# Kernel optimization log

Hardware: AMD Instinct MI355X
Metric: run time of the kernel (lower is better)

The kernel has to match this reference:

```python
import jax, jax.numpy as jnp
import numpy as np

D = 1024       # d_model
H = 16         # num_heads
DK = D // H    # head dim (64)
DFF = 4096     # SwiGLU hidden dim
THETA = 10000.0
EPS = 1e-5
B, S = 2, 2048


def setup_inputs() -> dict:
    key = jax.random.key(0)
    ks = jax.random.split(key, 9)
    p = lambda k, shape: jax.random.normal(k, shape, dtype=jnp.float32) * 0.02
    return {
        "x": jax.random.normal(ks[0], (B, S, D), dtype=jnp.float32),
        "w_q": p(ks[1], (D, D)),   # Linear stores [out, in]
        "w_k": p(ks[2], (D, D)),
        "w_v": p(ks[3], (D, D)),
        "w_o": p(ks[4], (D, D)),
        "ln1_w": jnp.ones((D,), dtype=jnp.float32),
        "ln2_w": jnp.ones((D,), dtype=jnp.float32),
        "w1": p(ks[5], (DFF, D)),  # gate-in proj: d_model -> dff
        "w2": p(ks[6], (D, DFF)),  # down proj:    dff -> d_model
        "w3": p(ks[7], (DFF, D)),  # up proj:      d_model -> dff
    }


def _rmsnorm(x, w):
    xf = x.astype(jnp.float32)
    inv = jax.lax.rsqrt(jnp.mean(xf * xf, axis=-1, keepdims=True) + EPS)
    return (inv * xf * w).astype(x.dtype)


def _rope(x, pos):
    # x: [..., seq, DK]; pos: [seq]
    inv_freq = THETA ** (-(jnp.arange(0, DK, 2, dtype=jnp.float32) / DK))  # [DK/2]
    ang = pos.astype(jnp.float32)[:, None] * inv_freq                      # [seq, DK/2]
    cos, sin = jnp.cos(ang), jnp.sin(ang)
    xe, xo = x[..., ::2], x[..., 1::2]
    re = cos * xe - sin * xo
    ro = sin * xe + cos * xo
    return jnp.stack((re, ro), axis=-1).reshape(x.shape)  # interleave even/odd


def reference(x, w_q, w_k, w_v, w_o, ln1_w, ln2_w, w1, w2, w3):
    b, s, d = x.shape
    pos = jnp.arange(s)

    # --- attention sublayer ---
    h = _rmsnorm(x, ln1_w)
    def proj(w):  # [b,s,d] x [d,d] -> [b,H,s,DK]
        return jnp.einsum('bsd,ed->bse', h, w).reshape(b, s, H, DK).transpose(0, 2, 1, 3)
    q = _rope(proj(w_q), pos)
    k = _rope(proj(w_k), pos)
    v = proj(w_v)

    scores = jnp.einsum('bhqd,bhkd->bhqk', q, k) / (DK ** 0.5)
    causal = jnp.tril(jnp.ones((s, s), dtype=bool))
    scores = jnp.where(causal, scores, -jnp.inf)
    attn = jax.nn.softmax(scores, axis=-1)
    o = jnp.einsum('bhqk,bhkd->bhqd', attn, v).transpose(0, 2, 1, 3).reshape(b, s, d)
    x = x + jnp.einsum('bsd,ed->bse', o, w_o)

    # --- SwiGLU FFN sublayer ---
    h2 = _rmsnorm(x, ln2_w)
    u = jnp.einsum('bsd,fd->bsf', h2, w1)
    g = jnp.einsum('bsd,fd->bsf', h2, w3)
    ffn = jnp.einsum('bsf,df->bsd', u * jax.nn.sigmoid(u) * g, w2)
    return x + ffn
```

## Files before the change

kernel.cpp:

```cpp
#include <hip/hip_runtime.h>

typedef _Float16 half_t;
typedef _Float16 f16x8 __attribute__((ext_vector_type(8)));
typedef _Float16 f16x4 __attribute__((ext_vector_type(4)));
typedef _Float16 f16x2 __attribute__((ext_vector_type(2)));
typedef float fx4 __attribute__((ext_vector_type(4)));

typedef __attribute__((address_space(1))) const unsigned int as1_cuint;
typedef __attribute__((address_space(3))) unsigned int as3_uint;

__device__ __forceinline__ void gld16(const void* g, void* l) {
    __builtin_amdgcn_global_load_lds((as1_cuint*)g, (as3_uint*)l, 16, 0, 0);
}

#define L256(buf, half, sec) (lbase + (buf) * 65536 + (half) * 16384 + (sec) * 8192)

#define KT256(CUR)                                                            \
  {                                                                           \
    const int BO = (CUR) * 65536;                                             \
    const int st1 = (t < nt - 1), st2 = (t < nt - 2);                         \
    const int s1 = (t + 1) * 128, s2 = (t + 2) * 128;                         \
    f16x8 aLo[4][2], aHi[4][2], bA[2][2], bB[2][2];                           \
                                         \
    _Pragma("unroll") for (int mi = 0; mi < 4; mi++) {                        \
        aLo[mi][0] = *(const f16x8*)(aBase + BO + mi * 2048 + swz0);          \
        aLo[mi][1] = *(const f16x8*)(aBase + BO + mi * 2048 + swz1);          \
    }                                                                         \
    _Pragma("unroll") for (int ni = 0; ni < 2; ni++) {                        \
        bA[ni][0] = *(const f16x8*)(bBase + BO + ni * 2048 + swz0);           \
        bA[ni][1] = *(const f16x8*)(bBase + BO + ni * 2048 + swz1);           \
    }                                                                         \
    if (st1) { gld16(pB10 + s1, L256(1 - (CUR), 3, 0));                       \
               gld16(pB1h + s1, L256(1 - (CUR), 3, 1)); }                     \
    asm volatile("s_waitcnt lgkmcnt(8)" ::: "memory");                        \
    __builtin_amdgcn_s_barrier();                                             \
    asm volatile("s_waitcnt lgkmcnt(0)" ::: "memory");                        \
    __builtin_amdgcn_sched_barrier(0);                                        \
    __builtin_amdgcn_s_setprio(1);                                            \
    _Pragma("unroll") for (int kk = 0; kk < 2; kk++)                          \
      _Pragma("unroll") for (int mi = 0; mi < 4; mi++)                        \
        _Pragma("unroll") for (int ni = 0; ni < 2; ni++)                      \
          acc[mi][ni] = __builtin_amdgcn_mfma_f32_16x16x32_f16(aLo[mi][kk], bA[ni][kk], acc[mi][ni], 0, 0, 0); \
    __builtin_amdgcn_s_setprio(0);                                            \
    __builtin_amdgcn_s_barrier();                                             \
                                         \
    _Pragma("unroll") for (int ni = 0; ni < 2; ni++) {                        \
        bB[ni][0] = *(const f16x8*)(bBase + BO + (2 + ni) * 2048 + swz0);     \
        bB[ni][1] = *(const f16x8*)(bBase + BO + (2 + ni) * 2048 + swz1);     \
    }                                                                         \
    if (st2) { gld16(pA00 + s2, L256(CUR, 0, 0)); }                           \
    __builtin_amdgcn_s_barrier();                                             \
    asm volatile("s_waitcnt lgkmcnt(0)" ::: "memory");                        \
    __builtin_amdgcn_sched_barrier(0);                                        \
    __builtin_amdgcn_s_setprio(1);                                            \
    _Pragma("unroll") for (int kk = 0; kk < 2; kk++)                          \
      _Pragma("unroll") for (int mi = 0; mi < 4; mi++)                        \
        _Pragma("unroll") for (int ni = 0; ni < 2; ni++)                      \
          acc[mi][2 + ni] = __builtin_amdgcn_mfma_f32_16x16x32_f16(aLo[mi][kk], bB[ni][kk], acc[mi][2 + ni], 0, 0, 0); \
    __builtin_amdgcn_s_setprio(0);                                            \
    __builtin_amdgcn_s_barrier();                                             \
                                         \
    _Pragma("unroll") for (int mi = 0; mi < 4; mi++) {                        \
        aHi[mi][0] = *(const f16x8*)(aBase + BO + (4 + mi) * 2048 + swz0);    \
        aHi[mi][1] = *(const f16x8*)(aBase + BO + (4 + mi) * 2048 + swz1);    \
    }                                                                         \
    if (st2) { gld16(pB00 + s2, L256(CUR, 2, 0));                             \
               gld16(pB0h + s2, L256(CUR, 2, 1)); }                           \
    __builtin_amdgcn_s_barrier();                                             \
    asm volatile("s_waitcnt lgkmcnt(0)" ::: "memory");                        \
    __builtin_amdgcn_sched_barrier(0);                                        \
    __builtin_amdgcn_s_setprio(1);                                            \
    _Pragma("unroll") for (int kk = 0; kk < 2; kk++)                          \
      _Pragma("unroll") for (int mi = 0; mi < 4; mi++)                        \
        _Pragma("unroll") for (int ni = 0; ni < 2; ni++)                      \
          acc[4 + mi][2 + ni] = __builtin_amdgcn_mfma_f32_16x16x32_f16(aHi[mi][kk], bB[ni][kk], acc[4 + mi][2 + ni], 0, 0, 0); \
    __builtin_amdgcn_s_setprio(0);                                            \
    __builtin_amdgcn_s_barrier();                                             \
                                         \
    if (st2) { gld16(pA0h + s2, L256(CUR, 0, 1));                             \
               gld16(pA10 + s2, L256(CUR, 1, 0));                             \
               gld16(pA1h + s2, L256(CUR, 1, 1)); }                           \
    __builtin_amdgcn_s_barrier();                                             \
    __builtin_amdgcn_sched_barrier(0);                                        \
    __builtin_amdgcn_s_setprio(1);                                            \
    _Pragma("unroll") for (int kk = 0; kk < 2; kk++)                          \
      _Pragma("unroll") for (int mi = 0; mi < 4; mi++)                        \
        _Pragma("unroll") for (int ni = 0; ni < 2; ni++)                      \
          acc[4 + mi][ni] = __builtin_amdgcn_mfma_f32_16x16x32_f16(aHi[mi][kk], bA[ni][kk], acc[4 + mi][ni], 0, 0, 0); \
    __builtin_amdgcn_s_setprio(0);                                            \
    if (t < nt - 2)       { asm volatile("s_waitcnt vmcnt(6)" ::: "memory"); }\
    else if (t == nt - 2) { asm volatile("s_waitcnt vmcnt(0)" ::: "memory"); }\
    __builtin_amdgcn_s_barrier();                                             \
  }

#define PRO256()                                                              \
    gld16(pA00, L256(0, 0, 0));                                               \
    gld16(pB00, L256(0, 2, 0)); gld16(pB0h, L256(0, 2, 1));                   \
    gld16(pA0h, L256(0, 0, 1)); gld16(pA10, L256(0, 1, 0)); gld16(pA1h, L256(0, 1, 1)); \
    gld16(pB10, L256(0, 3, 0)); gld16(pB1h, L256(0, 3, 1));                   \
    gld16(pA00 + 128, L256(1, 0, 0));                                         \
    gld16(pB00 + 128, L256(1, 2, 0)); gld16(pB0h + 128, L256(1, 2, 1));       \
    gld16(pA0h + 128, L256(1, 0, 1)); gld16(pA10 + 128, L256(1, 1, 0)); gld16(pA1h + 128, L256(1, 1, 1)); \
    asm volatile("s_waitcnt vmcnt(6)" ::: "memory");                          \
    __builtin_amdgcn_s_barrier();

template<int MODE>
__global__ __launch_bounds__(512, 2)
void gemm256(const half_t* __restrict__ A,
             const half_t* __restrict__ B0, const half_t* __restrict__ B1,
             const half_t* __restrict__ B2,
             half_t* o0, half_t* o1, half_t* o2, half_t* o3,
             int M, int N, int K)
{
    __shared__ half_t smem[65536];
    const int tid = threadIdx.x;
    const int wid = tid >> 6, lane = tid & 63;
    const int lm = lane & 15, lg = lane >> 4;
    const int wr = wid >> 2, wc = wid & 3;
    const int m0 = blockIdx.x * 256, n0 = blockIdx.y * 256;

    const half_t* Bp = B0;
    half_t* outb = o0;
    if (MODE == 1) {
        if (blockIdx.z == 1) { Bp = B1; outb = o1; }
        else if (blockIdx.z == 2) { Bp = B2; outb = o2; }
    }
    if (MODE == 4) {
        if (blockIdx.z == 1) outb = o1;
        else if (blockIdx.z == 2) outb = o2;
        else if (blockIdx.z == 3) outb = o3;
    }
    int Keff = K, koff = 0;
    if (MODE == 4) { Keff = K / gridDim.z; koff = blockIdx.z * Keff; }
    const int nt = Keff >> 6;

    const size_t KB = (size_t)K * 2;
    const int srow = tid >> 3;
    const int schunk = (tid & 7) ^ (srow & 7);
    const char* pA = (const char*)A + (size_t)(m0 + srow) * KB + (size_t)koff * 2 + schunk * 16;
    const char* pB = (const char*)Bp + (size_t)(n0 + srow) * KB + (size_t)koff * 2 + schunk * 16;
    const char* pA00 = pA;
    const char* pA0h = pA + 64 * KB;
    const char* pA10 = pA + 128 * KB;
    const char* pA1h = pA + 192 * KB;
    const char* pB00 = pB;
    const char* pB0h = pB + 64 * KB;
    const char* pB10 = pB + 128 * KB;
    const char* pB1h = pB + 192 * KB;

    char* const lbase = (char*)smem + tid * 16;

    const int swz0 = ((lg ^ (lm & 7)) << 4);
    const int swz1 = (((4 + lg) ^ (lm & 7)) << 4);
    const char* aBase = (const char*)smem + wr * 16384 + lm * 128;
    const char* bBase = (const char*)smem + (2 + (wc >> 1)) * 16384 + (wc & 1) * 8192 + lm * 128;

    PRO256()

    fx4 acc[8][4] = {};

#pragma unroll 1
    for (int tt = 0; tt < nt; tt += 2) {
        { const int t = tt;     KT256(0) }
        { const int t = tt + 1; KT256(1) }
    }

#pragma unroll
    for (int mi = 0; mi < 8; mi++) {
#pragma unroll
        for (int ni = 0; ni < 4; ni++) {
#pragma unroll
            for (int r = 0; r < 4; r++) {
                int m = m0 + wr * 128 + mi * 16 + lg * 4 + r;
                int n = n0 + wc * 64 + ni * 16 + lm;
                float v = acc[mi][ni][r];
                if (MODE == 1) {
                    int b = m >> 11, s = m & 2047, hh = n >> 6, dk = n & 63;
                    if (blockIdx.z == 2) {
                        outb[((size_t)(b * 16 + hh) * 64 + dk) * 2048 + s] = (half_t)v;
                    } else {
                        float pv = __shfl_xor(v, 1);
                        float f = __expf((float)(dk >> 1) * -0.28782313662f);
                        float c, sn;
                        __sincosf((float)s * f, &sn, &c);
                        float xe = (lm & 1) ? pv : v;
                        float xo = (lm & 1) ? v : pv;
                        float rv = (lm & 1) ? (sn * xe + c * xo) : (c * xe - sn * xo);
                        if (blockIdx.z == 0) rv *= 0.125f;
                        outb[((size_t)(b * 16 + hh) * 2048 + s) * 64 + dk] = (half_t)rv;
                    }
                } else {
                    outb[(size_t)m * N + n] = (half_t)v;
                }
            }
        }
    }
}

__global__ __launch_bounds__(512, 2)
void gemm_dual9(const half_t* __restrict__ A,
                const half_t* __restrict__ B1, const half_t* __restrict__ B2,
                half_t* __restrict__ out, int M, int N, int K)
{
    __shared__ half_t smem[65536];
    const int tid = threadIdx.x;
    const int wid = tid >> 6, lane = tid & 63;
    const int lm = lane & 15, lg = lane >> 4;
    const int wr = wid >> 2, wc = wid & 3;
    const int flat = blockIdx.x + (blockIdx.y << 4);
    const int wg = (flat & 7) * 64 + (flat >> 3);
    const int m0 = (wg & 15) * 256, n0 = (wg >> 4) * 128;

    const size_t KB = (size_t)K * 2;
    const int srow = tid >> 3;
    const int schunk = (tid & 7) ^ (srow & 7);
    const char* pA  = (const char*)A  + (size_t)(m0 + srow) * KB + schunk * 16;
    const char* pB0 = (const char*)B1 + (size_t)(n0 + srow) * KB + schunk * 16;
    const char* pB1 = (const char*)B2 + (size_t)(n0 + srow) * KB + schunk * 16;
    const char* pA00 = pA;
    const char* pA0h = pA + 64 * KB;
    const char* pA10 = pA + 128 * KB;
    const char* pA1h = pA + 192 * KB;
    const char* pB00 = pB0;
    const char* pB0h = pB0 + 64 * KB;
    const char* pB10 = pB1;
    const char* pB1h = pB1 + 64 * KB;
    const int nt = 16;

    char* const lbase = (char*)smem + tid * 16;

    const int swz0 = ((lg ^ (lm & 7)) << 4);
    const int swz1 = (((4 + lg) ^ (lm & 7)) << 4);
    const char* aBase = (const char*)smem + wr * 16384 + lm * 128;
    const char* bBase = (const char*)smem + (2 + (wc >> 1)) * 16384 + (wc & 1) * 8192 + lm * 128;

    PRO256()

    fx4 acc[8][4] = {};

#pragma unroll 1
    for (int tt = 0; tt < 16; tt += 2) {
        { const int t = tt;     KT256(0) }
        { const int t = tt + 1; KT256(1) }
    }

    float* gb = (float*)smem;
    if (wc >= 2) {
        const int gw = wr * 2 + (wc - 2);
#pragma unroll
        for (int mi = 0; mi < 8; mi++)
#pragma unroll
            for (int ni = 0; ni < 4; ni++)
                *(fx4*)((char*)gb + ((((gw * 8 + mi) * 4 + ni) * 64 + lane) << 4)) = acc[mi][ni];
    }
    __syncthreads();
    if (wc < 2) {
        const int gw = wr * 2 + wc;
#pragma unroll
        for (int mi = 0; mi < 8; mi++)
#pragma unroll
            for (int ni = 0; ni < 4; ni++) {
                fx4 gv = *(const fx4*)((const char*)gb + ((((gw * 8 + mi) * 4 + ni) * 64 + lane) << 4));
#pragma unroll
                for (int r = 0; r < 4; r++) {
                    int m = m0 + wr * 128 + mi * 16 + lg * 4 + r;
                    int n = n0 + wc * 64 + ni * 16 + lm;
                    float u = acc[mi][ni][r], g = gv[r];
                    out[(size_t)m * N + n] = (half_t)(u / (1.f + __expf(-u)) * g);
                }
            }
    }
}

__global__ __launch_bounds__(256, 4)
void addnorm_k(const float* __restrict__ x,
               const half_t* __restrict__ p0, const half_t* __restrict__ p1,
               const half_t* __restrict__ p2, const half_t* __restrict__ p3,
               const float* __restrict__ w,
               float* __restrict__ outF, half_t* __restrict__ outH)
{
    int row = blockIdx.x * 4 + (threadIdx.x >> 6);
    int lane = threadIdx.x & 63;
    const float4* xr = (const float4*)(x + (size_t)row * 1024);
    const f16x4* p0r = (const f16x4*)(p0 + (size_t)row * 1024);
    const f16x4* p1r = (const f16x4*)(p1 + (size_t)row * 1024);
    const f16x4* p2r = (const f16x4*)(p2 + (size_t)row * 1024);
    const f16x4* p3r = (const f16x4*)(p3 + (size_t)row * 1024);
    float4 v[4];
    float s = 0.f;
#pragma unroll
    for (int i = 0; i < 4; i++) {
        float4 xv = xr[lane + 64 * i];
        f16x4 a0 = p0r[lane + 64 * i];
        f16x4 a1 = p1r[lane + 64 * i];
        f16x4 a2 = p2r[lane + 64 * i];
        f16x4 a3 = p3r[lane + 64 * i];
        v[i].x = xv.x + (float)a0[0] + (float)a1[0] + (float)a2[0] + (float)a3[0];
        v[i].y = xv.y + (float)a0[1] + (float)a1[1] + (float)a2[1] + (float)a3[1];
        v[i].z = xv.z + (float)a0[2] + (float)a1[2] + (float)a2[2] + (float)a3[2];
        v[i].w = xv.w + (float)a0[3] + (float)a1[3] + (float)a2[3] + (float)a3[3];
        s += v[i].x * v[i].x + v[i].y * v[i].y + v[i].z * v[i].z + v[i].w * v[i].w;
    }
#pragma unroll
    for (int o = 32; o > 0; o >>= 1) s += __shfl_xor(s, o);
    float inv = rsqrtf(s * (1.f / 1024.f) + 1e-5f);
    const float4* w4 = (const float4*)w;
    float4* oF = (float4*)(outF + (size_t)row * 1024);
    f16x4* oH = (f16x4*)(outH + (size_t)row * 1024);
#pragma unroll
    for (int i = 0; i < 4; i++) {
        oF[lane + 64 * i] = v[i];
        float4 wv = w4[lane + 64 * i];
        f16x4 ov = { (half_t)(v[i].x * inv * wv.x), (half_t)(v[i].y * inv * wv.y),
                     (half_t)(v[i].z * inv * wv.z), (half_t)(v[i].w * inv * wv.w) };
        oH[lane + 64 * i] = ov;
    }
}

__global__ __launch_bounds__(256, 8)
void reduce4_k(const half_t* __restrict__ p0, const half_t* __restrict__ p1,
               const half_t* __restrict__ p2, const half_t* __restrict__ p3,
               float* __restrict__ out, int n4)
{
    int i = blockIdx.x * 256 + threadIdx.x;
    if (i >= n4) return;
    float4 b = ((const float4*)out)[i];
    f16x4 a0 = ((const f16x4*)p0)[i];
    f16x4 a1 = ((const f16x4*)p1)[i];
    f16x4 a2 = ((const f16x4*)p2)[i];
    f16x4 a3 = ((const f16x4*)p3)[i];
    float4 o = { b.x + (float)a0[0] + (float)a1[0] + (float)a2[0] + (float)a3[0],
                 b.y + (float)a0[1] + (float)a1[1] + (float)a2[1] + (float)a3[1],
                 b.z + (float)a0[2] + (float)a1[2] + (float)a2[2] + (float)a3[2],
                 b.w + (float)a0[3] + (float)a1[3] + (float)a2[3] + (float)a3[3] };
    ((float4*)out)[i] = o;
}

struct CastA { const float* s; half_t* d; int n4; };
struct CastArgs { CastA a[7]; };

__global__ __launch_bounds__(256)
void cast_rms_k(CastArgs ca, const float* __restrict__ x,
                const float* __restrict__ w, half_t* __restrict__ out)
{
    if (blockIdx.y < 7) {
        CastA a = ca.a[blockIdx.y];
        int i = blockIdx.x * 256 + threadIdx.x;
        if (i >= a.n4) return;
        float4 v = ((const float4*)a.s)[i];
        ((f16x4*)a.d)[i] = (f16x4){ (half_t)v.x, (half_t)v.y, (half_t)v.z, (half_t)v.w };
        return;
    }
    if (blockIdx.x >= 1024) return;
    int row = blockIdx.x * 4 + (threadIdx.x >> 6);
    int lane = threadIdx.x & 63;
    const float4* xr = (const float4*)(x + (size_t)row * 1024);
    float4 v[4];
    float s = 0.f;
#pragma unroll
    for (int i = 0; i < 4; i++) {
        v[i] = xr[lane + 64 * i];
        s += v[i].x * v[i].x + v[i].y * v[i].y + v[i].z * v[i].z + v[i].w * v[i].w;
    }
#pragma unroll
    for (int o = 32; o > 0; o >>= 1) s += __shfl_xor(s, o);
    float inv = rsqrtf(s * (1.f / 1024.f) + 1e-5f);
    const float4* w4 = (const float4*)w;
    f16x4* o4 = (f16x4*)(out + (size_t)row * 1024);
#pragma unroll
    for (int i = 0; i < 4; i++) {
        float4 wv = w4[lane + 64 * i];
        f16x4 ov = { (half_t)(v[i].x * inv * wv.x), (half_t)(v[i].y * inv * wv.y),
                     (half_t)(v[i].z * inv * wv.z), (half_t)(v[i].w * inv * wv.w) };
        o4[lane + 64 * i] = ov;
    }
}

__global__ __launch_bounds__(256, 2)
void attn_k(const half_t* __restrict__ Q, const half_t* __restrict__ K,
            const half_t* __restrict__ VT, half_t* __restrict__ O)
{
    __shared__ half_t sK[128 * 64];
    __shared__ half_t sVT[64 * 128];
    __shared__ half_t sP[4][16 * 128];
    const int tid = threadIdx.x, wid = tid >> 6, lane = tid & 63;
    const int lm = lane & 15, lg = lane >> 4;
    const int flat = blockIdx.x + (blockIdx.y << 4);
    const int wg = (flat & 7) * 64 + (flat >> 3);
    const int p = wg & 15, bh = wg >> 4;
    const int b = bh >> 4, hh = bh & 15;
    const size_t base = (size_t)bh * (2048 * 64);

    const int krow = tid >> 3;
    const int kcsw = ((tid & 7) ^ (krow & 7)) << 4;
    const int vrow = tid >> 4;
    const int vcsw = ((tid & 15) ^ (vrow & 15)) << 4;
    const char* gK = (const char*)(K + base);
    const char* gV = (const char*)(VT + base);
    char* lK = (char*)sK + tid * 16;
    char* lV = (char*)sVT + tid * 16;
    half_t* sPw = sP[wid];

    f16x8 vone;
#pragma unroll
    for (int j = 0; j < 8; j++) vone[j] = (half_t)1.f;

    for (int ph = 0; ph < 2; ph++) {
        const int qt = ph ? (31 - p) : p;
        const int q0 = qt * 64 + wid * 16;
        const int nT = (qt + 2) >> 1;

        f16x8 bQ[2];
#pragma unroll
        for (int ki = 0; ki < 2; ki++)
            bQ[ki] = *(const f16x8*)(Q + base + (size_t)(q0 + lm) * 64 + ki * 32 + lg * 8);

        fx4 oacc[4] = {};
        fx4 lacc = {};

        for (int t = 0; t < nT; t++) {
            const int kv0 = t * 128;
#pragma unroll
            for (int i = 0; i < 4; i++)
                gld16(gK + (size_t)(kv0 + i * 32 + krow) * 128 + kcsw, lK + i * 4096);
#pragma unroll
            for (int i = 0; i < 4; i++)
                gld16(gV + (size_t)(i * 16 + vrow) * 4096 + (size_t)kv0 * 2 + vcsw, lV + i * 4096);
            __syncthreads();

            fx4 st[8] = {};
#pragma unroll
            for (int ki = 0; ki < 2; ki++) {
#pragma unroll
                for (int mi = 0; mi < 8; mi++) {
                    f16x8 aK = *(const f16x8*)(sK + ((mi * 16 + lm) << 6) +
                                               (((ki * 4 + lg) ^ (lm & 7)) << 3));
                    st[mi] = __builtin_amdgcn_mfma_f32_16x16x32_f16(aK, bQ[ki], st[mi], 0, 0, 0);
                }
            }

            const bool diag = (t == nT - 1);
            const int qg = q0 + lm;
#pragma unroll
            for (int mi = 0; mi < 8; mi++) {
                f16x4 ev;
#pragma unroll
                for (int r = 0; r < 4; r++) {
                    float e = __expf(st[mi][r]);
                    if (diag && (kv0 + mi * 16 + lg * 4 + r > qg)) e = 0.f;
                    ev[r] = (half_t)e;
                }
                *(f16x4*)(sPw + (lm << 7) +
                          ((((mi * 2 + (lg >> 1)) ^ lm) << 3) | ((lg & 1) << 2))) = ev;
            }

#pragma unroll
            for (int k2 = 0; k2 < 4; k2++) {
                f16x8 aP = *(const f16x8*)(sPw + (lm << 7) + (((k2 * 4 + lg) ^ lm) << 3));
#pragma unroll
                for (int ni = 0; ni < 4; ni++) {
                    f16x8 bV = *(const f16x8*)(sVT + ((ni * 16 + lm) << 7) +
                                               (((k2 * 4 + lg) ^ lm) << 3));
                    oacc[ni] = __builtin_amdgcn_mfma_f32_16x16x32_f16(aP, bV, oacc[ni], 0, 0, 0);
                }
                lacc = __builtin_amdgcn_mfma_f32_16x16x32_f16(aP, vone, lacc, 0, 0, 0);
            }
            __syncthreads();
        }

        float inv[4];
#pragma unroll
        for (int r = 0; r < 4; r++) inv[r] = 1.f / lacc[r];
#pragma unroll
        for (int ni = 0; ni < 4; ni++)
#pragma unroll
            for (int r = 0; r < 4; r++) {
                int s = q0 + lg * 4 + r;
                O[((size_t)b * 2048 + s) * 1024 + hh * 64 + ni * 16 + lm] =
                    (half_t)(oacc[ni][r] * inv[r]);
            }
    }
}

extern "C" void kernel_launch(void* const* d_in, const int* in_sizes, int n_in,
                              void* d_out, int out_size, void* d_ws, size_t ws_size,
                              hipStream_t stream)
{
    const float* x   = (const float*)d_in[0];
    const float* wq  = (const float*)d_in[1];
    const float* wk  = (const float*)d_in[2];
    const float* wv  = (const float*)d_in[3];
    const float* wo  = (const float*)d_in[4];
    const float* ln1 = (const float*)d_in[5];
    const float* ln2 = (const float*)d_in[6];
    const float* w1  = (const float*)d_in[7];
    const float* w2  = (const float*)d_in[8];
    const float* w3  = (const float*)d_in[9];

    half_t* W = (half_t*)d_ws;
    const size_t Mi = 1048576;
    half_t* wq16 = W;
    half_t* wk16 = W + Mi;
    half_t* wv16 = W + 2 * Mi;
    half_t* wo16 = W + 3 * Mi;
    half_t* w116 = W + 4 * Mi;
    half_t* w316 = W + 8 * Mi;
    half_t* w216 = W + 12 * Mi;
    half_t* h16  = W + 16 * Mi;
    half_t* q16  = W + 20 * Mi;
    half_t* k16  = W + 24 * Mi;
    half_t* vt16 = W + 28 * Mi;
    half_t* a16  = W + 16 * Mi;
    half_t* h216 = W + 32 * Mi;
    half_t* P0   = W + 20 * Mi;
    half_t* P1   = W + 24 * Mi;
    half_t* P2   = W + 28 * Mi;
    half_t* P3   = W + 36 * Mi;
    half_t* D0   = W;
    half_t* D1   = W + 4 * Mi;
    half_t* D2   = W + 8 * Mi;
    half_t* D3   = W + 36 * Mi;

    CastArgs ca;
    ca.a[0] = { wq, wq16, 262144 };
    ca.a[1] = { wk, wk16, 262144 };
    ca.a[2] = { wv, wv16, 262144 };
    ca.a[3] = { wo, wo16, 262144 };
    ca.a[4] = { w1, w116, 1048576 };
    ca.a[5] = { w2, w216, 1048576 };
    ca.a[6] = { w3, w316, 1048576 };

    cast_rms_k<<<dim3(4096, 8), 256, 0, stream>>>(ca, x, ln1, h16);
    gemm256<1><<<dim3(16, 4, 3), 512, 0, stream>>>(h16, wq16, wk16, wv16,
                                                   q16, k16, vt16, nullptr,
                                                   4096, 1024, 1024);
    attn_k<<<dim3(16, 32), 256, 0, stream>>>(q16, k16, vt16, h16);
    gemm256<4><<<dim3(16, 4, 4), 512, 0, stream>>>(h16, wo16, nullptr, nullptr,
                                                   P0, P1, P2, P3,
                                                   4096, 1024, 1024);
    addnorm_k<<<dim3(1024), 256, 0, stream>>>(x, P0, P1, P2, P3, ln2,
                                              (float*)d_out, h216);
    gemm_dual9<<<dim3(16, 32), 512, 0, stream>>>(h216, w116, w316, a16,
                                                 4096, 4096, 1024);
    gemm256<4><<<dim3(16, 4, 4), 512, 0, stream>>>(a16, w216, nullptr, nullptr,
                                                   D0, D1, D2, D3,
                                                   4096, 1024, 4096);
    reduce4_k<<<dim3(4096), 256, 0, stream>>>(D0, D1, D2, D3, (float*)d_out, 1048576);
    (void)in_sizes; (void)n_in; (void)out_size; (void)ws_size;
}
```

Baseline: 388.9 us.

## Replace pipelined 256x256 GEMM with simple 128x128 tile GEMM, halve O-proj split-K

Removes the hand-pipelined 256x256 double-buffered gemm256 kernel and substitutes a simpler 128x128-tile, 256-thread GEMM with K-step 32 and no software pipelining. Grids grow from 16x4 to 32x8 tiles, raising block count and occupancy on the many-CU GPU. The output projection split-K drops from 4 to 2, so addnorm reads two partials instead of four. The new kernel syncs twice per K-step with no load/compute overlap and reuses less data per tile, so per-block efficiency may drop.

```diff
diff --git a/kernel.cpp b/kernel.cpp
--- a/kernel.cpp
+++ b/kernel.cpp
@@ -11,6 +11,104 @@
 
 __device__ __forceinline__ void gld16(const void* g, void* l) {
     __builtin_amdgcn_global_load_lds((as1_cuint*)g, (as3_uint*)l, 16, 0, 0);
+}
+
+template<int MODE>
+__global__ __launch_bounds__(256, 2)
+void gemm_bt(const half_t* __restrict__ A,
+             const half_t* __restrict__ B0, const half_t* __restrict__ B1,
+             const half_t* __restrict__ B2,
+             half_t* o0, half_t* o1, half_t* o2, half_t* o3,
+             int M, int N, int K)
+{
+    __shared__ half_t sA[128 * 32];
+    __shared__ half_t sB[128 * 32];
+    const int tid = threadIdx.x;
+    const int wid = tid >> 6, lane = tid & 63;
+    const int lm = lane & 15, lg = lane >> 4;
+    const int wr = wid >> 1, wc = wid & 1;
+    const int m0 = blockIdx.x * 128, n0 = blockIdx.y * 128;
+
+    const half_t* Bp = B0;
+    half_t* outb = o0;
+    if (MODE == 1) {
+        if (blockIdx.z == 1) { Bp = B1; outb = o1; }
+        else if (blockIdx.z == 2) { Bp = B2; outb = o2; }
+    }
+    if (MODE == 4) {
+        if (blockIdx.z == 1) outb = o1;
+        else if (blockIdx.z == 2) outb = o2;
+        else if (blockIdx.z == 3) outb = o3;
+    }
+
+    int Keff = K, koff = 0;
+    if (MODE == 4) { Keff = K / gridDim.z; koff = blockIdx.z * Keff; }
+
+    const int srow = tid >> 2;
+    const int scolb = ((tid & 3) ^ ((srow >> 1) & 3)) << 4;
+    const char* gA = (const char*)(A + (size_t)(m0 + srow) * K + koff) + scolb;
+    const char* gB = (const char*)(Bp + (size_t)(n0 + srow) * K + koff) + scolb;
+    const size_t rstep = (size_t)64 * K * sizeof(half_t);
+    char* lA = (char*)sA + tid * 16;
+    char* lB = (char*)sB + tid * 16;
+
+    const int ksw = (lm >> 1) & 3;
+
+    fx4 acc[4][4] = {};
+
+    for (int kt = 0; kt < Keff; kt += 32) {
+        gld16(gA, lA);
+        gld16(gA + rstep, lA + 4096);
+        gld16(gB, lB);
+        gld16(gB + rstep, lB + 4096);
+        gA += 64; gB += 64;
+        __syncthreads();
+        f16x8 aF[4], bF[4];
+#pragma unroll
+        for (int mi = 0; mi < 4; mi++)
+            aF[mi] = *(const f16x8*)(sA + (wr * 64 + mi * 16 + lm) * 32 + (lg ^ ksw) * 8);
+#pragma unroll
+        for (int ni = 0; ni < 4; ni++)
+            bF[ni] = *(const f16x8*)(sB + (wc * 64 + ni * 16 + lm) * 32 + (lg ^ ksw) * 8);
+#pragma unroll
+        for (int mi = 0; mi < 4; mi++)
+#pragma unroll
+            for (int ni = 0; ni < 4; ni++)
+                acc[mi][ni] = __builtin_amdgcn_mfma_f32_16x16x32_f16(aF[mi], bF[ni], acc[mi][ni], 0, 0, 0);
+        __syncthreads();
+    }
+
+#pragma unroll
+    for (int mi = 0; mi < 4; mi++) {
+#pragma unroll
+        for (int ni = 0; ni < 4; ni++) {
+#pragma unroll
+            for (int r = 0; r < 4; r++) {
+                int m = m0 + wr * 64 + mi * 16 + lg * 4 + r;
+                int n = n0 + wc * 64 + ni * 16 + lm;
+                float v = acc[mi][ni][r];
+                size_t idx = (size_t)m * N + n;
+                if (MODE == 1) {
+                    int b = m >> 11, s = m & 2047, hh = n >> 6, dk = n & 63;
+                    if (blockIdx.z == 2) {
+                        outb[((size_t)(b * 16 + hh) * 64 + dk) * 2048 + s] = (half_t)v;
+                    } else {
+                        float pv = __shfl_xor(v, 1);
+                        float f = __expf((float)(dk >> 1) * -0.28782313662f);
+                        float c, sn;
+                        __sincosf((float)s * f, &sn, &c);
+                        float xe = (lm & 1) ? pv : v;
+                        float xo = (lm & 1) ? v : pv;
+                        float rv = (lm & 1) ? (sn * xe + c * xo) : (c * xe - sn * xo);
+                        if (blockIdx.z == 0) rv *= 0.125f;
+                        outb[((size_t)(b * 16 + hh) * 2048 + s) * 64 + dk] = (half_t)rv;
+                    }
+                } else {
+                    outb[idx] = (half_t)v;
+                }
+            }
+        }
+    }
 }
 
 #define L256(buf, half, sec) (lbase + (buf) * 65536 + (half) * 16384 + (sec) * 8192)
@@ -104,99 +202,6 @@
     asm volatile("s_waitcnt vmcnt(6)" ::: "memory");                          \
     __builtin_amdgcn_s_barrier();
 
-template<int MODE>
-__global__ __launch_bounds__(512, 2)
-void gemm256(const half_t* __restrict__ A,
-             const half_t* __restrict__ B0, const half_t* __restrict__ B1,
-             const half_t* __restrict__ B2,
-             half_t* o0, half_t* o1, half_t* o2, half_t* o3,
-             int M, int N, int K)
-{
-    __shared__ half_t smem[65536];
-    const int tid = threadIdx.x;
-    const int wid = tid >> 6, lane = tid & 63;
-    const int lm = lane & 15, lg = lane >> 4;
-    const int wr = wid >> 2, wc = wid & 3;
-    const int m0 = blockIdx.x * 256, n0 = blockIdx.y * 256;
-
-    const half_t* Bp = B0;
-    half_t* outb = o0;
-    if (MODE == 1) {
-        if (blockIdx.z == 1) { Bp = B1; outb = o1; }
-        else if (blockIdx.z == 2) { Bp = B2; outb = o2; }
-    }
-    if (MODE == 4) {
-        if (blockIdx.z == 1) outb = o1;
-        else if (blockIdx.z == 2) outb = o2;
-        else if (blockIdx.z == 3) outb = o3;
-    }
-    int Keff = K, koff = 0;
-    if (MODE == 4) { Keff = K / gridDim.z; koff = blockIdx.z * Keff; }
-    const int nt = Keff >> 6;
-
-    const size_t KB = (size_t)K * 2;
-    const int srow = tid >> 3;
-    const int schunk = (tid & 7) ^ (srow & 7);
-    const char* pA = (const char*)A + (size_t)(m0 + srow) * KB + (size_t)koff * 2 + schunk * 16;
-    const char* pB = (const char*)Bp + (size_t)(n0 + srow) * KB + (size_t)koff * 2 + schunk * 16;
-    const char* pA00 = pA;
-    const char* pA0h = pA + 64 * KB;
-    const char* pA10 = pA + 128 * KB;
-    const char* pA1h = pA + 192 * KB;
-    const char* pB00 = pB;
-    const char* pB0h = pB + 64 * KB;
-    const char* pB10 = pB + 128 * KB;
-    const char* pB1h = pB + 192 * KB;
-
-    char* const lbase = (char*)smem + tid * 16;
-
-    const int swz0 = ((lg ^ (lm & 7)) << 4);
-    const int swz1 = (((4 + lg) ^ (lm & 7)) << 4);
-    const char* aBase = (const char*)smem + wr * 16384 + lm * 128;
-    const char* bBase = (const char*)smem + (2 + (wc >> 1)) * 16384 + (wc & 1) * 8192 + lm * 128;
-
-    PRO256()
-
-    fx4 acc[8][4] = {};
-
-#pragma unroll 1
-    for (int tt = 0; tt < nt; tt += 2) {
-        { const int t = tt;     KT256(0) }
-        { const int t = tt + 1; KT256(1) }
-    }
-
-#pragma unroll
-    for (int mi = 0; mi < 8; mi++) {
-#pragma unroll
-        for (int ni = 0; ni < 4; ni++) {
-#pragma unroll
-            for (int r = 0; r < 4; r++) {
-                int m = m0 + wr * 128 + mi * 16 + lg * 4 + r;
-                int n = n0 + wc * 64 + ni * 16 + lm;
-                float v = acc[mi][ni][r];
-                if (MODE == 1) {
-                    int b = m >> 11, s = m & 2047, hh = n >> 6, dk = n & 63;
-                    if (blockIdx.z == 2) {
-                        outb[((size_t)(b * 16 + hh) * 64 + dk) * 2048 + s] = (half_t)v;
-                    } else {
-                        float pv = __shfl_xor(v, 1);
-                        float f = __expf((float)(dk >> 1) * -0.28782313662f);
-                        float c, sn;
-                        __sincosf((float)s * f, &sn, &c);
-                        float xe = (lm & 1) ? pv : v;
-                        float xo = (lm & 1) ? v : pv;
-                        float rv = (lm & 1) ? (sn * xe + c * xo) : (c * xe - sn * xo);
-                        if (blockIdx.z == 0) rv *= 0.125f;
-                        outb[((size_t)(b * 16 + hh) * 2048 + s) * 64 + dk] = (half_t)rv;
-                    }
-                } else {
-                    outb[(size_t)m * N + n] = (half_t)v;
-                }
-            }
-        }
-    }
-}
-
 __global__ __launch_bounds__(512, 2)
 void gemm_dual9(const half_t* __restrict__ A,
                 const half_t* __restrict__ B1, const half_t* __restrict__ B2,
@@ -275,7 +280,6 @@
 __global__ __launch_bounds__(256, 4)
 void addnorm_k(const float* __restrict__ x,
                const half_t* __restrict__ p0, const half_t* __restrict__ p1,
-               const half_t* __restrict__ p2, const half_t* __restrict__ p3,
                const float* __restrict__ w,
                float* __restrict__ outF, half_t* __restrict__ outH)
 {
@@ -284,8 +288,6 @@
     const float4* xr = (const float4*)(x + (size_t)row * 1024);
     const f16x4* p0r = (const f16x4*)(p0 + (size_t)row * 1024);
     const f16x4* p1r = (const f16x4*)(p1 + (size_t)row * 1024);
-    const f16x4* p2r = (const f16x4*)(p2 + (size_t)row * 1024);
-    const f16x4* p3r = (const f16x4*)(p3 + (size_t)row * 1024);
     float4 v[4];
     float s = 0.f;
 #pragma unroll
@@ -293,12 +295,10 @@
         float4 xv = xr[lane + 64 * i];
         f16x4 a0 = p0r[lane + 64 * i];
         f16x4 a1 = p1r[lane + 64 * i];
-        f16x4 a2 = p2r[lane + 64 * i];
-        f16x4 a3 = p3r[lane + 64 * i];
-        v[i].x = xv.x + (float)a0[0] + (float)a1[0] + (float)a2[0] + (float)a3[0];
-        v[i].y = xv.y + (float)a0[1] + (float)a1[1] + (float)a2[1] + (float)a3[1];
-        v[i].z = xv.z + (float)a0[2] + (float)a1[2] + (float)a2[2] + (float)a3[2];
-        v[i].w = xv.w + (float)a0[3] + (float)a1[3] + (float)a2[3] + (float)a3[3];
+        v[i].x = xv.x + (float)a0[0] + (float)a1[0];
+        v[i].y = xv.y + (float)a0[1] + (float)a1[1];
+        v[i].z = xv.z + (float)a0[2] + (float)a1[2];
+        v[i].w = xv.w + (float)a0[3] + (float)a1[3];
         s += v[i].x * v[i].x + v[i].y * v[i].y + v[i].z * v[i].z + v[i].w * v[i].w;
     }
 #pragma unroll
@@ -514,8 +514,6 @@
     half_t* h216 = W + 32 * Mi;
     half_t* P0   = W + 20 * Mi;
     half_t* P1   = W + 24 * Mi;
-    half_t* P2   = W + 28 * Mi;
-    half_t* P3   = W + 36 * Mi;
     half_t* D0   = W;
     half_t* D1   = W + 4 * Mi;
     half_t* D2   = W + 8 * Mi;
@@ -531,18 +529,18 @@
     ca.a[6] = { w3, w316, 1048576 };
 
     cast_rms_k<<<dim3(4096, 8), 256, 0, stream>>>(ca, x, ln1, h16);
-    gemm256<1><<<dim3(16, 4, 3), 512, 0, stream>>>(h16, wq16, wk16, wv16,
+    gemm_bt<1><<<dim3(32, 8, 3), 256, 0, stream>>>(h16, wq16, wk16, wv16,
                                                    q16, k16, vt16, nullptr,
                                                    4096, 1024, 1024);
     attn_k<<<dim3(16, 32), 256, 0, stream>>>(q16, k16, vt16, h16);
-    gemm256<4><<<dim3(16, 4, 4), 512, 0, stream>>>(h16, wo16, nullptr, nullptr,
-                                                   P0, P1, P2, P3,
+    gemm_bt<4><<<dim3(32, 8, 2), 256, 0, stream>>>(h16, wo16, nullptr, nullptr,
+                                                   P0, P1, nullptr, nullptr,
                                                    4096, 1024, 1024);
-    addnorm_k<<<dim3(1024), 256, 0, stream>>>(x, P0, P1, P2, P3, ln2,
+    addnorm_k<<<dim3(1024), 256, 0, stream>>>(x, P0, P1, ln2,
                                               (float*)d_out, h216);
     gemm_dual9<<<dim3(16, 32), 512, 0, stream>>>(h216, w116, w316, a16,
                                                  4096, 4096, 1024);
-    gemm256<4><<<dim3(16, 4, 4), 512, 0, stream>>>(a16, w216, nullptr, nullptr,
+    gemm_bt<4><<<dim3(32, 8, 4), 256, 0, stream>>>(a16, w216, nullptr, nullptr,
                                                    D0, D1, D2, D3,
                                                    4096, 1024, 4096);
     reduce4_k<<<dim3(4096), 256, 0, stream>>>(D0, D1, D2, D3, (float*)d_out, 1048576);
```

After: 367.0 us, median of 2. -5.6%, faster.
